# Optimization experiments

Hardware: AMD Instinct MI355X
Metric: run time of the kernel (lower is better)

## Reference

```python
import jax, jax.numpy as jnp
import numpy as np

N = 8192
STATE_DIM = 64
HIDDENS = [512, 512]
LATENT = 128
TEMP = 1.0
EPS = 1e-12  # torch F.normalize eps


def _linear_params(key, fan_in, fan_out):
    k1, k2 = jax.random.split(key)
    bound = 1.0 / np.sqrt(fan_in)
    W = jax.random.uniform(k1, (fan_in, fan_out), jnp.float32, -bound, bound)
    b = jax.random.uniform(k2, (fan_out,), jnp.float32, -bound, bound)
    return W, b


def setup_inputs() -> dict:
    key = jax.random.key(0)
    ks = jax.random.split(key, 6)
    x = jax.random.normal(ks[0], (N, STATE_DIM), jnp.float32)
    y = jax.random.normal(ks[1], (N, STATE_DIM), jnp.float32)
    # state encoder params (forward uses state_enc for both x and y, as in source)
    W1, b1 = _linear_params(ks[2], STATE_DIM, HIDDENS[0])
    W2, b2 = _linear_params(ks[3], HIDDENS[0], HIDDENS[1])
    W3, b3 = _linear_params(ks[4], HIDDENS[1], LATENT)
    return {"x": x, "y": y, "W1": W1, "b1": b1, "W2": W2, "b2": b2, "W3": W3, "b3": b3}


def _encode(h, W1, b1, W2, b2, W3, b3):
    h = jax.nn.relu(h @ W1 + b1)
    h = jax.nn.relu(h @ W2 + b2)
    return h @ W3 + b3


def _l2norm(z):
    # matches torch F.normalize(dim=-1): z / max(||z||, eps)
    n = jnp.sqrt(jnp.sum(z * z, axis=-1, keepdims=True))
    return z / jnp.maximum(n, EPS)


def reference(x, y, W1, b1, W2, b2, W3, b3):
    zx = _l2norm(_encode(x, W1, b1, W2, b2, W3, b3))  # [N, LATENT]
    zy = _l2norm(_encode(y, W1, b1, W2, b2, W3, b3))  # [N, LATENT]
    # sum(x[:,None,:]*y[None,:,:], -1) == zx @ zy.T, expressed as tiled GEMM
    return jnp.einsum('id,jd->ij', zx, zy) / TEMP  # [N, N]
```

## Files before the change

### kernel.cpp

```cpp
#include <hip/hip_runtime.h>
#include <cstdint>
#include <cstddef>


typedef unsigned short u16;
typedef __attribute__((ext_vector_type(8))) short bf16x8;
typedef __attribute__((ext_vector_type(4))) float f32x4;
typedef __attribute__((ext_vector_type(4))) u16  u16x4;

__device__ __forceinline__ u16 f_to_bf16_bits(float f) {
    union { float f; uint32_t u; } v; v.f = f;
    uint32_t lsb = (v.u >> 16) & 1u;
    return (u16)((v.u + 0x7fffu + lsb) >> 16);
}

__global__ __launch_bounds__(256) void cast_inputs_kernel(
    const float* __restrict__ X, const float* __restrict__ Y,
    u16* __restrict__ xy)
{
    int i = blockIdx.x * 256 + threadIdx.x;
    float v = (i < 524288) ? X[i] : Y[i - 524288];
    xy[i] = f_to_bf16_bits(v);
}

__global__ __launch_bounds__(256) void transpose_weights_kernel(
    const float* __restrict__ W1, const float* __restrict__ W2,
    const float* __restrict__ W3,
    u16* __restrict__ W1T, u16* __restrict__ W2T, u16* __restrict__ W3T)
{
    int idx = blockIdx.x * 256 + threadIdx.x;
    if (idx < 32768) {
        int r = idx >> 9, c = idx & 511;
        W1T[c * 64 + r] = f_to_bf16_bits(W1[idx]);
    } else if (idx < 294912) {
        int k = idx - 32768;
        int r = k >> 9, c = k & 511;
        W2T[c * 512 + r] = f_to_bf16_bits(W2[k]);
    } else if (idx < 360448) {
        int k = idx - 294912;
        int r = k >> 7, c = k & 127;
        W3T[c * 512 + r] = f_to_bf16_bits(W3[k]);
    }
}

template<bool RELU>
__global__ __launch_bounds__(256) void gemm_lds_kernel(
    const u16* __restrict__ A, const u16* __restrict__ BT,
    const float* __restrict__ bias,
    u16* __restrict__ Cb,
    int M, int N, int K)
{
    __shared__ u16 lds[16 * 512];
    const int lane = threadIdx.x & 63;
    const int wave = threadIdx.x >> 6;
    const int wm = wave >> 1, wn = wave & 1;
    const int m_base = blockIdx.y * 128;
    const int n_base = blockIdx.x * 128;
    const int mi   = lane & 15;
    const int quad = lane >> 4;

    f32x4 acc[4][4];
    #pragma unroll
    for (int i = 0; i < 4; ++i)
        #pragma unroll
        for (int j = 0; j < 4; ++j)
            acc[i][j] = f32x4{0.f, 0.f, 0.f, 0.f};

    const u16* src[4];
    #pragma unroll
    for (int s = 0; s < 4; ++s) {
        const int t = wave * 4 + s;
        if (t < 8)
            src[s] = A + (size_t)(m_base + t * 16 + mi) * K + quad * 8;
        else
            src[s] = BT + (size_t)(n_base + (t - 8) * 16 + mi) * K + quad * 8;
    }
    u16* dst_base = &lds[wave * 4 * 512];

    for (int k0 = 0; k0 < K; k0 += 32) {
        #pragma unroll
        for (int s = 0; s < 4; ++s) {
            __builtin_amdgcn_global_load_lds(
                (const __attribute__((address_space(1))) void*)(src[s] + k0),
                (__attribute__((address_space(3))) void*)(dst_base + s * 512),
                16, 0, 0);
        }
        __syncthreads();

        bf16x8 af[4], bfr[4];
        #pragma unroll
        for (int i = 0; i < 4; ++i)
            af[i] = *reinterpret_cast<const bf16x8*>(&lds[(wm * 4 + i) * 512 + lane * 8]);
        #pragma unroll
        for (int j = 0; j < 4; ++j)
            bfr[j] = *reinterpret_cast<const bf16x8*>(&lds[(8 + wn * 4 + j) * 512 + lane * 8]);

        #pragma unroll
        for (int i = 0; i < 4; ++i)
            #pragma unroll
            for (int j = 0; j < 4; ++j)
                acc[i][j] = __builtin_amdgcn_mfma_f32_16x16x32_bf16(
                    af[i], bfr[j], acc[i][j], 0, 0, 0);

        __syncthreads();
    }

    const int wm_base = m_base + wm * 64;
    const int wn_base = n_base + wn * 64;
    #pragma unroll
    for (int j = 0; j < 4; ++j) {
        const int col = wn_base + j * 16 + mi;
        float bv = bias[col];
        #pragma unroll
        for (int i = 0; i < 4; ++i) {
            const int row0 = wm_base + i * 16 + quad * 4;
            #pragma unroll
            for (int r = 0; r < 4; ++r) {
                float v = acc[i][j][r] + bv;
                if (RELU) v = fmaxf(v, 0.f);
                Cb[(size_t)(row0 + r) * N + col] = f_to_bf16_bits(v);
            }
        }
    }
}

__global__ __launch_bounds__(256) void gemm3_l2norm_kernel(
    const u16* __restrict__ H2, const u16* __restrict__ W3T,
    const float* __restrict__ b3, u16* __restrict__ ZN)
{
    const int lane = threadIdx.x & 63;
    const int wave = threadIdx.x >> 6;
    const int mi   = lane & 15;
    const int quad = lane >> 4;
    const int grow = blockIdx.x * 64 + wave * 16 + mi;

    bf16x8 hf[16];
    const u16* hbase = H2 + (size_t)grow * 512 + quad * 8;
    #pragma unroll
    for (int ks = 0; ks < 16; ++ks)
        hf[ks] = *reinterpret_cast<const bf16x8*>(hbase + ks * 32);

    f32x4 zv[8];
    #pragma unroll
    for (int cb = 0; cb < 8; ++cb) zv[cb] = f32x4{0.f, 0.f, 0.f, 0.f};

    const u16* wbase = W3T + (size_t)mi * 512 + quad * 8;
    #pragma unroll 1
    for (int ks = 0; ks < 16; ++ks) {
        #pragma unroll
        for (int cb = 0; cb < 8; ++cb) {
            bf16x8 wf = *reinterpret_cast<const bf16x8*>(
                wbase + (size_t)cb * 16 * 512 + ks * 32);
            zv[cb] = __builtin_amdgcn_mfma_f32_16x16x32_bf16(wf, hf[ks], zv[cb], 0, 0, 0);
        }
    }

    float s = 0.f;
    #pragma unroll
    for (int cb = 0; cb < 8; ++cb) {
        const float* bp = b3 + cb * 16 + quad * 4;
        #pragma unroll
        for (int r = 0; r < 4; ++r) {
            zv[cb][r] += bp[r];
            s += zv[cb][r] * zv[cb][r];
        }
    }
    s += __shfl_xor(s, 16, 64);
    s += __shfl_xor(s, 32, 64);
    const float inv = 1.0f / fmaxf(sqrtf(s), 1e-12f);

    u16* zrow = ZN + (size_t)grow * 128;
    #pragma unroll
    for (int cb = 0; cb < 8; ++cb) {
        u16x4 pk;
        #pragma unroll
        for (int r = 0; r < 4; ++r) pk[r] = f_to_bf16_bits(zv[cb][r] * inv);
        *reinterpret_cast<u16x4*>(zrow + cb * 16 + quad * 4) = pk;
    }
}

__global__ __launch_bounds__(256) void gemm_nt_k128_kernel(
    const u16* __restrict__ ZX, const u16* __restrict__ ZY,
    float* __restrict__ out)
{
    const int lane = threadIdx.x & 63;
    const int wave = threadIdx.x >> 6;
    const int mi   = lane & 15;
    const int quad = lane >> 4;
    const int wr = wave >> 1, wc = wave & 1;
    const int rb = blockIdx.y * 128 + wr * 64;
    const int cb = blockIdx.x * 128 + wc * 64;

    f32x4 acc[4][4];
    #pragma unroll
    for (int ci = 0; ci < 4; ++ci)
        #pragma unroll
        for (int rj = 0; rj < 4; ++rj)
            acc[ci][rj] = f32x4{0.f, 0.f, 0.f, 0.f};

    const u16* xbase = ZX + (size_t)(rb + mi) * 128 + quad * 8;
    const u16* ybase = ZY + (size_t)(cb + mi) * 128 + quad * 8;

    #pragma unroll
    for (int ks = 0; ks < 4; ++ks) {
        bf16x8 yf[4], xf[4];
        #pragma unroll
        for (int t = 0; t < 4; ++t) {
            yf[t] = *reinterpret_cast<const bf16x8*>(ybase + (size_t)t * 16 * 128 + ks * 32);
            xf[t] = *reinterpret_cast<const bf16x8*>(xbase + (size_t)t * 16 * 128 + ks * 32);
        }
        #pragma unroll
        for (int ci = 0; ci < 4; ++ci)
            #pragma unroll
            for (int rj = 0; rj < 4; ++rj)
                acc[ci][rj] = __builtin_amdgcn_mfma_f32_16x16x32_bf16(
                    yf[ci], xf[rj], acc[ci][rj], 0, 0, 0);
    }

    #pragma unroll
    for (int rj = 0; rj < 4; ++rj) {
        float* orow = out + (size_t)(rb + rj * 16 + mi) * 8192 + cb + quad * 4;
        #pragma unroll
        for (int ci = 0; ci < 4; ++ci)
            *reinterpret_cast<f32x4*>(orow + ci * 16) = acc[ci][rj];
    }
}

extern "C" void kernel_launch(void* const* d_in, const int* in_sizes, int n_in,
                              void* d_out, int out_size, void* d_ws, size_t ws_size,
                              hipStream_t stream)
{
    const float* x  = (const float*)d_in[0];
    const float* y  = (const float*)d_in[1];
    const float* W1 = (const float*)d_in[2];
    const float* b1 = (const float*)d_in[3];
    const float* W2 = (const float*)d_in[4];
    const float* b2 = (const float*)d_in[5];
    const float* W3 = (const float*)d_in[6];
    const float* b3 = (const float*)d_in[7];
    float* out = (float*)d_out;

    u16* ws  = (u16*)d_ws;
    u16* xy  = ws;
    u16* W1T = xy  + (size_t)16384 * 64;
    u16* W2T = W1T + 512 * 64;
    u16* W3T = W2T + 512 * 512;
    u16* h1  = W3T + 128 * 512;
    u16* h2  = h1  + (size_t)16384 * 512;
    u16* zn  = h2  + (size_t)16384 * 512;

    dim3 blk(256);

    cast_inputs_kernel<<<4096, blk, 0, stream>>>(x, y, xy);

    transpose_weights_kernel<<<1408, blk, 0, stream>>>(
        W1, W2, W3, W1T, W2T, W3T);

    gemm_lds_kernel<true><<<dim3(4, 128), blk, 0, stream>>>(
        xy, W1T, b1, h1, 16384, 512, 64);
    gemm_lds_kernel<true><<<dim3(4, 128), blk, 0, stream>>>(
        h1, W2T, b2, h2, 16384, 512, 512);

    gemm3_l2norm_kernel<<<256, blk, 0, stream>>>(h2, W3T, b3, zn);

    gemm_nt_k128_kernel<<<dim3(64, 64), blk, 0, stream>>>(
        zn, zn + (size_t)8192 * 128, out);
}
```

Before: 376.9 us.

## Fuse input cast into first-layer GEMM and swizzle final GEMM block order

Removes the separate fp32-to-bf16 input cast kernel. The first encoder layer now reads x/y directly in fp32, converts in registers, and computes the K=64 GEMM with weights loaded straight from global memory, with bias and ReLU in the epilogue. The final 8192x8192 similarity GEMM remaps block indices so consecutive blocks cover different row tiles, aiming at better L2 reuse of operands. Together these drop a launch and an intermediate buffer write/read, at the cost of an unshared, non-LDS weight load pattern in layer 1.

```diff
diff --git a/kernel.cpp b/kernel.cpp
--- a/kernel.cpp
+++ b/kernel.cpp
@@ -12,15 +12,6 @@
     union { float f; uint32_t u; } v; v.f = f;
     uint32_t lsb = (v.u >> 16) & 1u;
     return (u16)((v.u + 0x7fffu + lsb) >> 16);
-}
-
-__global__ __launch_bounds__(256) void cast_inputs_kernel(
-    const float* __restrict__ X, const float* __restrict__ Y,
-    u16* __restrict__ xy)
-{
-    int i = blockIdx.x * 256 + threadIdx.x;
-    float v = (i < 524288) ? X[i] : Y[i - 524288];
-    xy[i] = f_to_bf16_bits(v);
 }
 
 __global__ __launch_bounds__(256) void transpose_weights_kernel(
@@ -43,7 +34,64 @@
     }
 }
 
-template<bool RELU>
+__global__ __launch_bounds__(256) void gemm1_direct_kernel(
+    const float* __restrict__ X, const float* __restrict__ Y,
+    const u16* __restrict__ W1T, const float* __restrict__ b1,
+    u16* __restrict__ H1)
+{
+    const int lane = threadIdx.x & 63;
+    const int wave = threadIdx.x >> 6;
+    const int mi   = lane & 15;
+    const int quad = lane >> 4;
+    const int wrh  = wave >> 1;
+    const int wch  = wave & 1;
+    const int grow = blockIdx.x * 32 + wrh * 16 + mi;
+    const float* srow = (grow < 8192) ? (X + (size_t)grow * 64)
+                                      : (Y + (size_t)(grow - 8192) * 64);
+
+    bf16x8 xf[2];
+    #pragma unroll
+    for (int ks = 0; ks < 2; ++ks) {
+        const float* p = srow + ks * 32 + quad * 8;
+        float4 f0 = *reinterpret_cast<const float4*>(p);
+        float4 f1 = *reinterpret_cast<const float4*>(p + 4);
+        union { u16 u[8]; bf16x8 v; } cv;
+        cv.u[0] = f_to_bf16_bits(f0.x); cv.u[1] = f_to_bf16_bits(f0.y);
+        cv.u[2] = f_to_bf16_bits(f0.z); cv.u[3] = f_to_bf16_bits(f0.w);
+        cv.u[4] = f_to_bf16_bits(f1.x); cv.u[5] = f_to_bf16_bits(f1.y);
+        cv.u[6] = f_to_bf16_bits(f1.z); cv.u[7] = f_to_bf16_bits(f1.w);
+        xf[ks] = cv.v;
+    }
+
+    u16* hrow = H1 + (size_t)grow * 512;
+    #pragma unroll 1
+    for (int cbg = 0; cbg < 4; ++cbg) {
+        f32x4 a[4];
+        #pragma unroll
+        for (int j = 0; j < 4; ++j) a[j] = f32x4{0.f, 0.f, 0.f, 0.f};
+        #pragma unroll
+        for (int j = 0; j < 4; ++j) {
+            const int cb = wch * 16 + cbg * 4 + j;
+            #pragma unroll
+            for (int ks = 0; ks < 2; ++ks) {
+                bf16x8 wf = *reinterpret_cast<const bf16x8*>(
+                    W1T + (size_t)(cb * 16 + mi) * 64 + ks * 32 + quad * 8);
+                a[j] = __builtin_amdgcn_mfma_f32_16x16x32_bf16(wf, xf[ks], a[j], 0, 0, 0);
+            }
+        }
+        #pragma unroll
+        for (int j = 0; j < 4; ++j) {
+            const int cb = wch * 16 + cbg * 4 + j;
+            const float* bp = b1 + cb * 16 + quad * 4;
+            u16x4 pk;
+            #pragma unroll
+            for (int r = 0; r < 4; ++r)
+                pk[r] = f_to_bf16_bits(fmaxf(a[j][r] + bp[r], 0.f));
+            *reinterpret_cast<u16x4*>(hrow + cb * 16 + quad * 4) = pk;
+        }
+    }
+}
+
 __global__ __launch_bounds__(256) void gemm_lds_kernel(
     const u16* __restrict__ A, const u16* __restrict__ BT,
     const float* __restrict__ bias,
@@ -116,8 +164,7 @@
             const int row0 = wm_base + i * 16 + quad * 4;
             #pragma unroll
             for (int r = 0; r < 4; ++r) {
-                float v = acc[i][j][r] + bv;
-                if (RELU) v = fmaxf(v, 0.f);
+                float v = fmaxf(acc[i][j][r] + bv, 0.f);
                 Cb[(size_t)(row0 + r) * N + col] = f_to_bf16_bits(v);
             }
         }
@@ -188,8 +235,11 @@
     const int mi   = lane & 15;
     const int quad = lane >> 4;
     const int wr = wave >> 1, wc = wave & 1;
-    const int rb = blockIdx.y * 128 + wr * 64;
-    const int cb = blockIdx.x * 128 + wc * 64;
+
+    const int orig = blockIdx.y * 64 + blockIdx.x;
+    const int swz  = (orig & 7) * 512 + (orig >> 3);
+    const int rb = (swz >> 6) * 128 + wr * 64;
+    const int cb = (swz & 63) * 128 + wc * 64;
 
     f32x4 acc[4][4];
     #pragma unroll
@@ -241,8 +291,7 @@
     float* out = (float*)d_out;
 
     u16* ws  = (u16*)d_ws;
-    u16* xy  = ws;
-    u16* W1T = xy  + (size_t)16384 * 64;
+    u16* W1T = ws;
     u16* W2T = W1T + 512 * 64;
     u16* W3T = W2T + 512 * 512;
     u16* h1  = W3T + 128 * 512;
@@ -251,14 +300,12 @@
 
     dim3 blk(256);
 
-    cast_inputs_kernel<<<4096, blk, 0, stream>>>(x, y, xy);
-
     transpose_weights_kernel<<<1408, blk, 0, stream>>>(
         W1, W2, W3, W1T, W2T, W3T);
 
-    gemm_lds_kernel<true><<<dim3(4, 128), blk, 0, stream>>>(
-        xy, W1T, b1, h1, 16384, 512, 64);
-    gemm_lds_kernel<true><<<dim3(4, 128), blk, 0, stream>>>(
+    gemm1_direct_kernel<<<512, blk, 0, stream>>>(x, y, W1T, b1, h1);
+
+    gemm_lds_kernel<<<dim3(4, 128), blk, 0, stream>>>(
         h1, W2T, b2, h2, 16384, 512, 512);
 
     gemm3_l2norm_kernel<<<256, blk, 0, stream>>>(h2, W3T, b3, zn);
```

New measurement: 378.7 us. Within noise of the previous version (+0.5%).
